# Performance work log

Measured on AMD Instinct MI355X. Metric: run time of the kernel, lower is better.

Reference implementation:

```python
import jax, jax.numpy as jnp
import numpy as np

DIM = 256
HID = 1024
BATCH = 16384
STEP_SIZE = 0.1
NSTEPS = 10  # int(1.0 / step_size)


def setup_inputs() -> dict:
    key = jax.random.key(0)
    ks = jax.random.split(key, 8)
    x = jax.random.normal(ks[0], (BATCH, DIM), dtype=jnp.float32)
    # Scaled init so tanh layers stay in a sane range (like default torch init).
    W1 = jax.random.normal(ks[1], (DIM + 1, HID), dtype=jnp.float32) / np.sqrt(DIM + 1)
    b1 = jnp.zeros((HID,), dtype=jnp.float32)
    W2 = jax.random.normal(ks[2], (HID, HID), dtype=jnp.float32) / np.sqrt(HID)
    b2 = jnp.zeros((HID,), dtype=jnp.float32)
    W3 = jax.random.normal(ks[3], (HID, DIM), dtype=jnp.float32) / np.sqrt(HID)
    b3 = jnp.zeros((DIM,), dtype=jnp.float32)
    proj_mat = jax.random.normal(ks[4], (DIM, DIM), dtype=jnp.float32)
    return {"x": x, "W1": W1, "b1": b1, "W2": W2, "b2": b2,
            "W3": W3, "b3": b3, "proj_mat": proj_mat}


def reference(x, W1, b1, W2, b2, W3, b3, proj_mat):
    """FlowProposal.log_prob: backward RK4 integration of dx/dt = v(x,t)
    from t=1 to t=0 with Hutchinson trace estimation via forward-mode JVP.
    Returns log q(x), shape [batch]."""
    dtype = x.dtype

    def net(xc, t):
        # VelocityMLP: concat(x, t) -> tanh MLP -> velocity [B, DIM]
        tcol = jnp.broadcast_to(jnp.asarray(t, dtype), (xc.shape[0], 1))
        h = jnp.tanh(jnp.concatenate([xc, tcol], axis=1) @ W1 + b1)
        h = jnp.tanh(h @ W2 + b2)
        return h @ W3 + b3

    # Deterministic hashed Hutchinson noise (from the INITIAL x, as in torch).
    noise = jnp.sin((x @ proj_mat) * 1000.0) * 1.41421356  # sqrt(2)

    def dyn(xc, t):
        v, jv = jax.jvp(lambda xi: net(xi, t), (xc,), (noise,))
        tr = jnp.sum(noise * jv, axis=1, keepdims=True)  # eps^T J eps, [B,1]
        return v, tr

    dt = -STEP_SIZE

    def step(carry, k):
        xt, ljt = carry
        t = 1.0 + dt * k
        v1, tr1 = dyn(xt, t)
        v2, tr2 = dyn(xt + dt * 0.5 * v1, t + dt * 0.5)
        v3, tr3 = dyn(xt + dt * 0.5 * v2, t + dt * 0.5)
        v4, tr4 = dyn(xt + dt * v3, t + dt)
        xt = xt + (dt / 6.0) * (v1 + 2 * v2 + 2 * v3 + v4)
        ljt = ljt + (dt / 6.0) * (tr1 + 2 * tr2 + 2 * tr3 + tr4)
        return (xt, ljt), None

    init = (x, jnp.zeros((x.shape[0], 1), dtype))
    (xt, ljt), _ = jax.lax.scan(step, init, jnp.arange(NSTEPS, dtype=dtype))

    log_prob_z = -0.5 * jnp.sum(xt * xt, axis=1) - 0.5 * DIM * jnp.log(jnp.asarray(2.0 * np.pi, dtype))
    return log_prob_z - ljt[:, 0]
```

## Files before the change

### kernel.cpp

```cpp
#include <hip/hip_runtime.h>
#include <stdint.h>
#include <stddef.h>

typedef unsigned short ushort_t;
typedef float f32x4 __attribute__((ext_vector_type(4)));
typedef short short8 __attribute__((ext_vector_type(8)));

#define NB 16384
#define DIMX 256
#define HIDX 1024
#define DTC (-0.1f)

__device__ __forceinline__ unsigned short f2bf_bits(float f){
  unsigned int u = __float_as_uint(f);
  unsigned int r = (u + 0x7FFFu + ((u >> 16) & 1u)) >> 16;
  return (unsigned short)r;
}
__device__ __forceinline__ float bf2f_bits(unsigned short s){
  return __uint_as_float(((unsigned int)s) << 16);
}
__device__ __forceinline__ float fast_tanh(float x){
  float a = fabsf(x);
  float e = __expf(a + a);
  float r = 1.0f - 2.0f / (e + 1.0f);
  return copysignf(r, x);
}
__device__ __forceinline__ void gload16(const void* g, void* l){
  __builtin_amdgcn_global_load_lds(
      (const __attribute__((address_space(1))) void*)g,
      (__attribute__((address_space(3))) void*)l, 16, 0, 0);
}
template<int N> __device__ __forceinline__ void wait_vmcnt(){
  if constexpr (N == 0)      asm volatile("s_waitcnt vmcnt(0)" ::: "memory");
  else if constexpr (N == 4) asm volatile("s_waitcnt vmcnt(4)" ::: "memory");
  else if constexpr (N == 8) asm volatile("s_waitcnt vmcnt(8)" ::: "memory");
  else static_assert(N == 0, "unsupported vmcnt");
}
__device__ __forceinline__ int ldsx(int r, int c){
  return r * 64 + (c ^ ((r & 7) << 3));
}
__device__ __forceinline__ int ldsx2(int r, int g){
  return r * 32 + ((g ^ ((r >> 1) & 3)) << 3);
}

__global__ void prep_weights(const float* __restrict__ W1, const float* __restrict__ W2,
                             const float* __restrict__ W3,
                             ushort_t* __restrict__ W1at, ushort_t* __restrict__ W2t,
                             ushort_t* __restrict__ W3t, ushort_t* __restrict__ W3n){
  int i = blockIdx.x * blockDim.x + threadIdx.x;
  const int T1 = 1024 * 256, T2 = 1024 * 1024, T3 = 256 * 1024, T4 = 1024 * 256;
  if (i < T1){
    int n = i >> 8, k = i & 255;
    W1at[i] = f2bf_bits(W1[k * 1024 + n]);
  } else if (i < T1 + T2){
    int j = i - T1; int n = j >> 10, k = j & 1023;
    W2t[j] = f2bf_bits(W2[k * 1024 + n]);
  } else if (i < T1 + T2 + T3){
    int j = i - T1 - T2; int n = j >> 10, k = j & 1023;
    W3t[j] = f2bf_bits(W3[k * 256 + n]);
  } else if (i < T1 + T2 + T3 + T4){
    int j = i - T1 - T2 - T3;
    W3n[j] = f2bf_bits(W3[j]);
  }
}

__global__ void noise_init(const float* __restrict__ x, const float* __restrict__ proj,
                           ushort_t* __restrict__ noise_bf,
                           float* __restrict__ xt, ushort_t* __restrict__ xcbf,
                           float* __restrict__ ljt){
  const int r0 = blockIdx.x * 8;
  const int j = threadIdx.x;
  __shared__ float xrow[8][256];
  #pragma unroll
  for (int r = 0; r < 8; ++r) xrow[r][j] = x[(size_t)(r0 + r) * 256 + j];
  __syncthreads();
  float s[8] = {0.f,0.f,0.f,0.f,0.f,0.f,0.f,0.f};
  for (int k = 0; k < 256; ++k){
    float p = proj[k * 256 + j];
    #pragma unroll
    for (int r = 0; r < 8; ++r) s[r] = fmaf(xrow[r][k], p, s[r]);
  }
  #pragma unroll
  for (int r = 0; r < 8; ++r){
    float nz = sinf(s[r] * 1000.0f) * 1.41421356237f;
    size_t idx = (size_t)(r0 + r) * 256 + j;
    noise_bf[idx] = f2bf_bits(nz);
    float xv = xrow[r][j];
    xt[idx] = xv;
    xcbf[idx] = f2bf_bits(xv);
  }
  if (j < 8) ljt[r0 + j] = 0.0f;
}

template<int BM, int BN, int WGM, int K, int DUAL, int EPI, int PIPE>
__launch_bounds__(512, 2)
__global__ void gemm_kernel(const ushort_t* __restrict__ A1, const ushort_t* __restrict__ A2,
                            const ushort_t* __restrict__ Wt,
                            ushort_t* __restrict__ out1, ushort_t* __restrict__ out2,
                            const float* __restrict__ bias, const float* __restrict__ w1trow,
                            float tval,
                            const ushort_t* __restrict__ dz1,
                            const ushort_t* __restrict__ gtr,
                            float* __restrict__ xt, float* __restrict__ vacc,
                            ushort_t* __restrict__ xcbf,
                            float* __restrict__ ljt, float wdt6, int rk){
  constexpr int WGN = 8 / WGM;
  constexpr int WM = BM / WGM, WN = BN / WGN;
  constexpr int M_REP = WM / 16, N_REP = WN / 16;
  constexpr int ATILES = DUAL ? 2 : 1;
  constexpr int ROWS = ATILES * BM + BN;

  const int m0 = blockIdx.x * BM;
  const int n0 = blockIdx.y * BN;
  const int tid = threadIdx.x;
  const int lane = tid & 63;
  const int wid = tid >> 6;
  const int wr = wid / WGN;
  const int wc = wid % WGN;

  f32x4 acc1[M_REP][N_REP] = {};
  f32x4 acc2[M_REP][N_REP] = {};

  if constexpr (PIPE == 2){
    constexpr int NT = K / 32;
    constexpr int CH = ROWS / 16;
    constexpr int CH_PW = CH / 8;
    constexpr int BUF_E = ROWS * 32;
    static_assert(CH_PW * 8 == CH, "chunk split");
    __shared__ __align__(16) ushort_t lds[4 * BUF_E];

    const int srow = lane >> 2;
    const int scol = (((lane & 3) ^ ((srow >> 1) & 3)) << 3);
    const ushort_t* srcb[CH_PW];
    #pragma unroll
    for (int c = 0; c < CH_PW; ++c){
      const int ch = wid * CH_PW + c;
      const int r = ch * 16 + srow;
      if (r < BM)            srcb[c] = A1 + (size_t)(m0 + r) * K + scol;
      else if (DUAL && r < 2 * BM) srcb[c] = A2 + (size_t)(m0 + r - BM) * K + scol;
      else                   srcb[c] = Wt + (size_t)(n0 + r - ATILES * BM) * K + scol;
    }
    auto do_stage = [&](int t){
      ushort_t* dst = lds + (t & 3) * BUF_E + (wid * CH_PW) * 512;
      #pragma unroll
      for (int c = 0; c < CH_PW; ++c)
        gload16(srcb[c] + t * 32, dst + c * 512);
    };

    do_stage(0); do_stage(1); do_stage(2);
    const int g = lane >> 4;
    const int lro = lane & 15;
    for (int t = 0; t < NT; ++t){
      asm volatile("s_waitcnt lgkmcnt(0)" ::: "memory");
      __builtin_amdgcn_s_barrier();
      if (t < NT - 2)       wait_vmcnt<8>();
      else if (t == NT - 2) wait_vmcnt<4>();
      else                  wait_vmcnt<0>();
      const ushort_t* base = lds + (t & 3) * BUF_E;
      short8 a1f[M_REP], a2f[M_REP], bfr[N_REP];
      #pragma unroll
      for (int m = 0; m < M_REP; ++m){
        int r = wr * WM + m * 16 + lro;
        a1f[m] = *(const short8*)(base + ldsx2(r, g));
        if (DUAL) a2f[m] = *(const short8*)(base + ldsx2(BM + r, g));
      }
      #pragma unroll
      for (int n = 0; n < N_REP; ++n){
        int cN = ATILES * BM + wc * WN + n * 16 + lro;
        bfr[n] = *(const short8*)(base + ldsx2(cN, g));
      }
      if (t + 3 < NT) do_stage(t + 3);
      __builtin_amdgcn_s_setprio(1);
      #pragma unroll
      for (int m = 0; m < M_REP; ++m){
        #pragma unroll
        for (int n = 0; n < N_REP; ++n){
          acc1[m][n] = __builtin_amdgcn_mfma_f32_16x16x32_bf16(a1f[m], bfr[n], acc1[m][n], 0, 0, 0);
          if (DUAL)
            acc2[m][n] = __builtin_amdgcn_mfma_f32_16x16x32_bf16(a2f[m], bfr[n], acc2[m][n], 0, 0, 0);
        }
      }
      __builtin_amdgcn_s_setprio(0);
    }
  } else {
    constexpr int BK = 64;
    constexpr int CH_A = BM / 8;
    constexpr int CH_TOT = ATILES * CH_A + BN / 8;
    constexpr int CH_PW = CH_TOT / 8;
    constexpr int BUF_E = ROWS * BK;
    constexpr int NK = K / BK;
    __shared__ __align__(16) ushort_t lds[BUF_E];

    const int srow = lane >> 3;
    const int scol = ((lane & 7) ^ srow) * 8;
    const ushort_t* srcb[CH_PW];
    #pragma unroll
    for (int c = 0; c < CH_PW; ++c){
      const int ch = wid * CH_PW + c;
      if (ch < CH_A)
        srcb[c] = A1 + (size_t)(m0 + ch * 8 + srow) * K + scol;
      else if (DUAL && ch < 2 * CH_A)
        srcb[c] = A2 + (size_t)(m0 + (ch - CH_A) * 8 + srow) * K + scol;
      else
        srcb[c] = Wt + (size_t)(n0 + (ch - ATILES * CH_A) * 8 + srow) * K + scol;
    }
    for (int ks = 0; ks < NK; ++ks){
      {
        ushort_t* dst = lds + (wid * CH_PW) * 512;
        #pragma unroll
        for (int c = 0; c < CH_PW; ++c)
          gload16(srcb[c] + ks * BK, dst + c * 512);
      }
      __syncthreads();
      const ushort_t* ldsA1 = lds;
      const ushort_t* ldsA2 = lds + BM * BK;
      const ushort_t* ldsB  = lds + ATILES * BM * BK;
      #pragma unroll
      for (int kk = 0; kk < 2; ++kk){
        short8 a1f[M_REP], a2f[M_REP], bfr[N_REP];
        const int lco = kk * 32 + (lane >> 4) * 8;
        const int lro = lane & 15;
        #pragma unroll
        for (int m = 0; m < M_REP; ++m){
          int r = wr * WM + m * 16 + lro;
          a1f[m] = *(const short8*)(ldsA1 + ldsx(r, lco));
          if (DUAL) a2f[m] = *(const short8*)(ldsA2 + ldsx(r, lco));
        }
        #pragma unroll
        for (int n = 0; n < N_REP; ++n){
          int cN = wc * WN + n * 16 + lro;
          bfr[n] = *(const short8*)(ldsB + ldsx(cN, lco));
        }
        #pragma unroll
        for (int m = 0; m < M_REP; ++m){
          #pragma unroll
          for (int n = 0; n < N_REP; ++n){
            acc1[m][n] = __builtin_amdgcn_mfma_f32_16x16x32_bf16(a1f[m], bfr[n], acc1[m][n], 0, 0, 0);
            if (DUAL)
              acc2[m][n] = __builtin_amdgcn_mfma_f32_16x16x32_bf16(a2f[m], bfr[n], acc2[m][n], 0, 0, 0);
          }
        }
      }
      __syncthreads();
    }
  }

  const int rbase = (lane >> 4) * 4;
  const int cbase = lane & 15;
  if (EPI <= 1){
    #pragma unroll
    for (int m = 0; m < M_REP; ++m){
      #pragma unroll
      for (int n = 0; n < N_REP; ++n){
        #pragma unroll
        for (int j = 0; j < 4; ++j){
          const int R = m0 + wr * WM + m * 16 + rbase + j;
          const int C = n0 + wc * WN + n * 16 + cbase;
          const size_t idx = (size_t)R * HIDX + C;
          float a = acc1[m][n][j];
          if (EPI == 0){
            out1[idx] = f2bf_bits(a);
          } else {
            float z = a + bias[C] + tval * w1trow[C];
            float h = fast_tanh(z);
            out1[idx] = f2bf_bits(h);
            float d = bf2f_bits(dz1[idx]);
            out2[idx] = f2bf_bits(fmaf(-h, h, 1.0f) * d);
          }
        }
      }
    }
  } else if (EPI == 2){
    #pragma unroll
    for (int m = 0; m < M_REP; ++m){
      #pragma unroll
      for (int j = 0; j < 4; ++j){
        const int R = m0 + wr * WM + m * 16 + rbase + j;
        float psum = 0.0f;
        #pragma unroll
        for (int n = 0; n < N_REP; ++n){
          const int C = n0 + wc * WN + n * 16 + cbase;
          const size_t idx = (size_t)R * HIDX + C;
          float h = fast_tanh(acc1[m][n][j] + bias[C]);
          out1[idx] = f2bf_bits(h);
          float dh2 = fmaf(-h, h, 1.0f) * acc2[m][n][j];
          psum += dh2 * bf2f_bits(gtr[idx]);
        }
        #pragma unroll
        for (int off = 1; off < 16; off <<= 1) psum += __shfl_xor(psum, off, 64);
        if (cbase == 0) atomicAdd(&ljt[R], wdt6 * psum);
      }
    }
  } else {
    #pragma unroll
    for (int m = 0; m < M_REP; ++m){
      #pragma unroll
      for (int n = 0; n < N_REP; ++n){
        #pragma unroll
        for (int j = 0; j < 4; ++j){
          const int R = m0 + wr * WM + m * 16 + rbase + j;
          const int C = n0 + wc * WN + n * 16 + cbase;
          const size_t idx = (size_t)R * DIMX + C;
          float v = acc1[m][n][j] + bias[C];
          float xtv = xt[idx];
          if (rk == 0){
            vacc[idx] = v;
            xcbf[idx] = f2bf_bits(xtv + 0.5f * DTC * v);
          } else if (rk == 1){
            vacc[idx] += 2.0f * v;
            xcbf[idx] = f2bf_bits(xtv + 0.5f * DTC * v);
          } else if (rk == 2){
            vacc[idx] += 2.0f * v;
            xcbf[idx] = f2bf_bits(xtv + DTC * v);
          } else {
            float xtn = xtv + (DTC / 6.0f) * (vacc[idx] + v);
            xt[idx] = xtn;
            xcbf[idx] = f2bf_bits(xtn);
          }
        }
      }
    }
  }
}

__global__ void final_kernel(const float* __restrict__ xt, const float* __restrict__ ljt,
                             float* __restrict__ out){
  const int row = blockIdx.x * 4 + (threadIdx.x >> 6);
  const int lane = threadIdx.x & 63;
  const float4 xv = *(const float4*)(xt + (size_t)row * 256 + lane * 4);
  float s = xv.x * xv.x + xv.y * xv.y + xv.z * xv.z + xv.w * xv.w;
  #pragma unroll
  for (int off = 32; off; off >>= 1) s += __shfl_xor(s, off, 64);
  if (lane == 0) out[row] = -0.5f * s - 235.2482645f - ljt[row];
}

extern "C" void kernel_launch(void* const* d_in, const int* in_sizes, int n_in,
                              void* d_out, int out_size, void* d_ws, size_t ws_size,
                              hipStream_t stream){
  (void)in_sizes; (void)n_in; (void)out_size; (void)ws_size;
  const float* x    = (const float*)d_in[0];
  const float* W1   = (const float*)d_in[1];
  const float* b1   = (const float*)d_in[2];
  const float* W2   = (const float*)d_in[3];
  const float* b2   = (const float*)d_in[4];
  const float* W3   = (const float*)d_in[5];
  const float* b3   = (const float*)d_in[6];
  const float* proj = (const float*)d_in[7];

  size_t off = 0;
  char* wsb = (char*)d_ws;
  auto carve = [&](size_t n) -> char* {
    char* p = wsb + off; off += (n + 255) & ~(size_t)255; return p;
  };
  ushort_t* W1at     = (ushort_t*)carve((size_t)1024 * 256 * 2);
  ushort_t* W2t      = (ushort_t*)carve((size_t)1024 * 1024 * 2);
  ushort_t* W3t      = (ushort_t*)carve((size_t)256 * 1024 * 2);
  ushort_t* W3n      = (ushort_t*)carve((size_t)1024 * 256 * 2);
  ushort_t* noise_bf = (ushort_t*)carve((size_t)NB * 256 * 2);
  ushort_t* dz1      = (ushort_t*)carve((size_t)NB * 1024 * 2);
  ushort_t* gtr      = (ushort_t*)carve((size_t)NB * 1024 * 2);
  float*    xt       = (float*)carve((size_t)NB * 256 * 4);
  ushort_t* xcbf     = (ushort_t*)carve((size_t)NB * 256 * 2);
  float*    vacc     = (float*)carve((size_t)NB * 256 * 4);
  float*    ljt      = (float*)carve((size_t)NB * 4);
  ushort_t* h1       = (ushort_t*)carve((size_t)NB * 1024 * 2);
  ushort_t* dh1      = (ushort_t*)carve((size_t)NB * 1024 * 2);
  ushort_t* h2       = (ushort_t*)carve((size_t)NB * 1024 * 2);

  prep_weights<<<7168, 256, 0, stream>>>(W1, W2, W3, W1at, W2t, W3t, W3n);
  noise_init<<<NB / 8, 256, 0, stream>>>(x, proj, noise_bf, xt, xcbf, ljt);

  gemm_kernel<256, 256, 2, 256, 0, 0, 0><<<dim3(NB / 256, 4), 512, 0, stream>>>(
      noise_bf, nullptr, W1at, dz1, nullptr, nullptr, nullptr, 0.f,
      nullptr, nullptr, nullptr, nullptr, nullptr, nullptr, 0.f, 0);
  gemm_kernel<256, 256, 2, 256, 0, 0, 0><<<dim3(NB / 256, 4), 512, 0, stream>>>(
      noise_bf, nullptr, W3n, gtr, nullptr, nullptr, nullptr, 0.f,
      nullptr, nullptr, nullptr, nullptr, nullptr, nullptr, 0.f, 0);

  const float toff[4] = {0.0f, -0.05f, -0.05f, -0.1f};
  const float wst[4]  = {1.0f, 2.0f, 2.0f, 1.0f};
  for (int k = 0; k < 10; ++k){
    float t = 1.0f - 0.1f * (float)k;
    for (int s = 0; s < 4; ++s){
      gemm_kernel<256, 256, 2, 256, 0, 1, 0><<<dim3(NB / 256, 4), 512, 0, stream>>>(
          xcbf, nullptr, W1at, h1, dh1, b1, W1 + 256 * 1024, t + toff[s],
          dz1, nullptr, nullptr, nullptr, nullptr, nullptr, 0.f, 0);
      gemm_kernel<128, 256, 2, 1024, 1, 2, 2><<<dim3(NB / 128, 4), 512, 0, stream>>>(
          h1, dh1, W2t, h2, nullptr, b2, nullptr, 0.f,
          nullptr, gtr, nullptr, nullptr, nullptr, ljt, wst[s] * (DTC / 6.0f), 0);
      gemm_kernel<128, 128, 4, 1024, 0, 3, 0><<<dim3(NB / 128, 2), 512, 0, stream>>>(
          h2, nullptr, W3t, nullptr, nullptr, b3, nullptr, 0.f,
          nullptr, nullptr, xt, vacc, xcbf, nullptr, 0.f, s);
    }
  }
  final_kernel<<<NB / 4, 256, 0, stream>>>(xt, ljt, (float*)d_out);
}
```

Before: 6.015 ms.

## Restructure dual-GEMM pipeline into half-tile staged loads interleaved with MFMA phases

Replaces the 4-deep BK=32 ring-buffer pipeline for the dual-A GEMM path with BK=64 tiles. A and B are double-buffered separately, and each K-step is split into four MFMA phases. Global-to-LDS loads for the next B tile and the A tile two steps ahead are issued in parts between phases, so memory traffic overlaps with compute. This uses the 8-row XOR swizzle layout and adds more barriers per iteration, trading extra synchronisation for finer-grained overlap. A static_assert restricts the path to a fixed 256x256 tile geometry.

New measurement: 5.621 ms. 1.07x faster.

```diff
diff --git a/kernel.cpp b/kernel.cpp
--- a/kernel.cpp
+++ b/kernel.cpp
@@ -38,9 +38,6 @@
 }
 __device__ __forceinline__ int ldsx(int r, int c){
   return r * 64 + (c ^ ((r & 7) << 3));
-}
-__device__ __forceinline__ int ldsx2(int r, int g){
-  return r * 32 + ((g ^ ((r >> 1) & 3)) << 3);
 }
 
 __global__ void prep_weights(const float* __restrict__ W1, const float* __restrict__ W2,
@@ -122,65 +119,111 @@
   f32x4 acc2[M_REP][N_REP] = {};
 
   if constexpr (PIPE == 2){
-    constexpr int NT = K / 32;
-    constexpr int CH = ROWS / 16;
-    constexpr int CH_PW = CH / 8;
-    constexpr int BUF_E = ROWS * 32;
-    static_assert(CH_PW * 8 == CH, "chunk split");
-    __shared__ __align__(16) ushort_t lds[4 * BUF_E];
-
-    const int srow = lane >> 2;
-    const int scol = (((lane & 3) ^ ((srow >> 1) & 3)) << 3);
-    const ushort_t* srcb[CH_PW];
-    #pragma unroll
-    for (int c = 0; c < CH_PW; ++c){
-      const int ch = wid * CH_PW + c;
-      const int r = ch * 16 + srow;
-      if (r < BM)            srcb[c] = A1 + (size_t)(m0 + r) * K + scol;
-      else if (DUAL && r < 2 * BM) srcb[c] = A2 + (size_t)(m0 + r - BM) * K + scol;
-      else                   srcb[c] = Wt + (size_t)(n0 + r - ATILES * BM) * K + scol;
-    }
-    auto do_stage = [&](int t){
-      ushort_t* dst = lds + (t & 3) * BUF_E + (wid * CH_PW) * 512;
-      #pragma unroll
-      for (int c = 0; c < CH_PW; ++c)
-        gload16(srcb[c] + t * 32, dst + c * 512);
+    static_assert(DUAL == 1 && ATILES * BM == 256 && BN == 256 && WGM == 2,
+                  "halftile geometry");
+    constexpr int NT = K / 64;
+    constexpr int HBUF_E = 256 * 64;
+    __shared__ __align__(16) ushort_t lds[4 * HBUF_E];
+
+    const int srow = lane >> 3;
+    const int scol = ((lane & 7) ^ srow) * 8;
+    const ushort_t* srcA0 = (wid < 4)
+        ? A1 + (size_t)(m0 + wid * 32 + srow) * K + scol
+        : A2 + (size_t)(m0 + wid * 32 - 128 + srow) * K + scol;
+    const ushort_t* srcB0 = Wt + (size_t)(n0 + wid * 32 + srow) * K + scol;
+
+    auto stageA = [&](int t, int part){
+      ushort_t* dst = lds + (t & 1) * HBUF_E + (wid * 4) * 512;
+      #pragma unroll
+      for (int c = 0; c < 2; ++c){
+        const int ch = 2 * part + c;
+        gload16(srcA0 + (size_t)ch * 8 * K + t * 64, dst + ch * 512);
+      }
     };
-
-    do_stage(0); do_stage(1); do_stage(2);
-    const int g = lane >> 4;
+    auto stageB = [&](int t, int part){
+      ushort_t* dst = lds + (2 + (t & 1)) * HBUF_E + (wid * 4) * 512;
+      #pragma unroll
+      for (int c = 0; c < 2; ++c){
+        const int ch = 2 * part + c;
+        gload16(srcB0 + (size_t)ch * 8 * K + t * 64, dst + ch * 512);
+      }
+    };
+    stageA(0, 0); stageA(0, 1); stageB(0, 0); stageB(0, 1);
+    stageA(1, 0); stageA(1, 1);
+
     const int lro = lane & 15;
+    const int lq8 = (lane >> 4) * 8;
     for (int t = 0; t < NT; ++t){
+      const ushort_t* ab = lds + (t & 1) * HBUF_E;
+      const ushort_t* bb = lds + (2 + (t & 1)) * HBUF_E;
+      short8 a1f[2][M_REP], a2f[2][M_REP], b0fr[N_REP], b1fr[N_REP];
+      if (t < NT - 1) wait_vmcnt<4>(); else wait_vmcnt<0>();
+      #pragma unroll
+      for (int m = 0; m < M_REP; ++m){
+        const int r = wr * WM + m * 16 + lro;
+        a1f[0][m] = *(const short8*)(ab + ldsx(r, lq8));
+        a1f[1][m] = *(const short8*)(ab + ldsx(r, 32 + lq8));
+      }
+      #pragma unroll
+      for (int n = 0; n < N_REP; ++n){
+        const int rn = wc * WN + n * 16 + lro;
+        b0fr[n] = *(const short8*)(bb + ldsx(rn, lq8));
+      }
+      if (t + 1 < NT) stageB(t + 1, 0);
+      __builtin_amdgcn_s_barrier();
       asm volatile("s_waitcnt lgkmcnt(0)" ::: "memory");
-      __builtin_amdgcn_s_barrier();
-      if (t < NT - 2)       wait_vmcnt<8>();
-      else if (t == NT - 2) wait_vmcnt<4>();
-      else                  wait_vmcnt<0>();
-      const ushort_t* base = lds + (t & 3) * BUF_E;
-      short8 a1f[M_REP], a2f[M_REP], bfr[N_REP];
+      __builtin_amdgcn_s_setprio(1);
+      #pragma unroll
+      for (int m = 0; m < M_REP; ++m)
+        #pragma unroll
+        for (int n = 0; n < N_REP; ++n)
+          acc1[m][n] = __builtin_amdgcn_mfma_f32_16x16x32_bf16(a1f[0][m], b0fr[n], acc1[m][n], 0, 0, 0);
+      __builtin_amdgcn_s_setprio(0);
+      __builtin_amdgcn_s_barrier();
       #pragma unroll
       for (int m = 0; m < M_REP; ++m){
-        int r = wr * WM + m * 16 + lro;
-        a1f[m] = *(const short8*)(base + ldsx2(r, g));
-        if (DUAL) a2f[m] = *(const short8*)(base + ldsx2(BM + r, g));
-      }
+        const int r = BM + wr * WM + m * 16 + lro;
+        a2f[0][m] = *(const short8*)(ab + ldsx(r, lq8));
+        a2f[1][m] = *(const short8*)(ab + ldsx(r, 32 + lq8));
+      }
+      if (t + 1 < NT) stageB(t + 1, 1);
+      __builtin_amdgcn_s_barrier();
+      asm volatile("s_waitcnt lgkmcnt(0)" ::: "memory");
+      __builtin_amdgcn_s_setprio(1);
+      #pragma unroll
+      for (int m = 0; m < M_REP; ++m)
+        #pragma unroll
+        for (int n = 0; n < N_REP; ++n)
+          acc2[m][n] = __builtin_amdgcn_mfma_f32_16x16x32_bf16(a2f[0][m], b0fr[n], acc2[m][n], 0, 0, 0);
+      __builtin_amdgcn_s_setprio(0);
+      __builtin_amdgcn_s_barrier();
       #pragma unroll
       for (int n = 0; n < N_REP; ++n){
-        int cN = ATILES * BM + wc * WN + n * 16 + lro;
-        bfr[n] = *(const short8*)(base + ldsx2(cN, g));
-      }
-      if (t + 3 < NT) do_stage(t + 3);
+        const int rn = wc * WN + n * 16 + lro;
+        b1fr[n] = *(const short8*)(bb + ldsx(rn, 32 + lq8));
+      }
+      if (t + 2 < NT) stageA(t + 2, 0);
+      __builtin_amdgcn_s_barrier();
+      asm volatile("s_waitcnt lgkmcnt(0)" ::: "memory");
       __builtin_amdgcn_s_setprio(1);
       #pragma unroll
-      for (int m = 0; m < M_REP; ++m){
-        #pragma unroll
-        for (int n = 0; n < N_REP; ++n){
-          acc1[m][n] = __builtin_amdgcn_mfma_f32_16x16x32_bf16(a1f[m], bfr[n], acc1[m][n], 0, 0, 0);
-          if (DUAL)
-            acc2[m][n] = __builtin_amdgcn_mfma_f32_16x16x32_bf16(a2f[m], bfr[n], acc2[m][n], 0, 0, 0);
-        }
-      }
+      for (int m = 0; m < M_REP; ++m)
+        #pragma unroll
+        for (int n = 0; n < N_REP; ++n)
+          acc1[m][n] = __builtin_amdgcn_mfma_f32_16x16x32_bf16(a1f[1][m], b1fr[n], acc1[m][n], 0, 0, 0);
       __builtin_amdgcn_s_setprio(0);
+      __builtin_amdgcn_s_barrier();
+      if (t + 2 < NT) stageA(t + 2, 1);
+      __builtin_amdgcn_s_barrier();
+      asm volatile("s_waitcnt lgkmcnt(0)" ::: "memory");
+      __builtin_amdgcn_s_setprio(1);
+      #pragma unroll
+      for (int m = 0; m < M_REP; ++m)
+        #pragma unroll
+        for (int n = 0; n < N_REP; ++n)
+          acc2[m][n] = __builtin_amdgcn_mfma_f32_16x16x32_bf16(a2f[1][m], b1fr[n], acc2[m][n], 0, 0, 0);
+      __builtin_amdgcn_s_setprio(0);
+      __builtin_amdgcn_s_barrier();
     }
   } else {
     constexpr int BK = 64;
```
